# Kernel tuning notes

Hardware: AMD Instinct MI355X
Metric: run time of the kernel (lower is better)

## Reference

```python
import jax, jax.numpy as jnp
import numpy as np

T, B, IN, H = 2048, 2048, 5, 10


def setup_inputs() -> dict:
    key = jax.random.key(0)
    ks = jax.random.split(key, 7)
    return {
        "x": jax.random.normal(ks[0], (T, B, IN), dtype=jnp.float32),
        "hx0": jax.random.uniform(ks[1], (B, H), dtype=jnp.float32),
        "cx0": jax.random.uniform(ks[2], (B, H), dtype=jnp.float32),
        "W_ih": jax.random.normal(ks[3], (4 * H, IN), dtype=jnp.float32) * 0.3,
        "W_hh": jax.random.normal(ks[4], (4 * H, H), dtype=jnp.float32) * 0.3,
        "b_ih": jax.random.normal(ks[5], (4 * H,), dtype=jnp.float32) * 0.1,
        "b_hh": jax.random.normal(ks[6], (4 * H,), dtype=jnp.float32) * 0.1,
    }


def reference(x, hx0, cx0, W_ih, W_hh, b_ih, b_hh):
    # torch.nn.LSTMCell gate order: i, f, g, o
    bias = b_ih + b_hh  # [4H]

    def step(carry, xt):
        h, c = carry  # [B, H] each
        gates = xt @ W_ih.T + h @ W_hh.T + bias  # [B, 4H]
        i, f, g, o = jnp.split(gates, 4, axis=-1)
        c_new = jax.nn.sigmoid(f) * c + jax.nn.sigmoid(i) * jnp.tanh(g)
        h_new = jax.nn.sigmoid(o) * jnp.tanh(c_new)
        return (h_new, c_new), h_new

    _, hs = jax.lax.scan(step, (hx0, cx0), x)  # hs: [T, B, H]
    # original concatenates per-step hx along dim 0 -> [T*B, H]
    return hs.reshape(-1, hs.shape[-1])
```

## Files before the change

### kernel.cpp

```cpp
#include <hip/hip_runtime.h>


#define T_STEPS 2048
#define BATCH   2048
#define NIN     5
#define NH      10
#define PF      8

__device__ __forceinline__ float hw_exp2(float v) { return __builtin_amdgcn_exp2f(v); }
__device__ __forceinline__ float hw_rcp(float v)  { return __builtin_amdgcn_rcpf(v); }

__global__ __launch_bounds__(64) void lstm_fused_kernel(
    const float* __restrict__ x,   const float* __restrict__ hx0,
    const float* __restrict__ cx0, const float* __restrict__ Wih,
    const float* __restrict__ Whh, const float* __restrict__ bih,
    const float* __restrict__ bhh, float* __restrict__ out)
{
    const float LOG2E = 1.4426950408889634f;

    const int lane = threadIdx.x;
    int grp = lane / 20;
    const bool act = (grp < 3);
    if (!act) grp = 2;
    int l2 = lane - grp * 20;
    if (l2 > 19) l2 = 19;
    const int j = l2 >> 1;
    const int p = l2 & 1;

    const int b    = blockIdx.x * 3 + grp;
    const bool bval = act && (b < BATCH);
    const int bl   = (b < BATCH) ? b : (BATCH - 1);

    const int row_a = p ? (2 * NH + j) : (NH + j);
    const int row_b = p ? (3 * NH + j) : j;

    float wa[NIN + NH], wb[NIN + NH];
#pragma unroll
    for (int k = 0; k < NIN; ++k) {
        wa[k] = Wih[row_a * NIN + k];
        wb[k] = Wih[row_b * NIN + k];
    }
#pragma unroll
    for (int k = 0; k < NH; ++k) {
        wa[NIN + k] = Whh[row_a * NH + k];
        wb[NIN + k] = Whh[row_b * NH + k];
    }
    const float bias_a = bih[row_a] + bhh[row_a];
    const float bias_b = bih[row_b] + bhh[row_b];

    const float ka = p ? (-2.0f * LOG2E) : (-LOG2E);
    const float Aa = p ? 2.0f : 1.0f;
    const float Ba = p ? -1.0f : 0.0f;

    float hv[NH];
#pragma unroll
    for (int k = 0; k < NH; ++k) hv[k] = hx0[bl * NH + k];
    float cst = cx0[bl * NH + j];

    const int srcbase = grp * 20;

    const float* xb = x + (size_t)bl * NIN;
    float xr[PF][NIN];
#pragma unroll
    for (int q = 0; q < PF; ++q) {
#pragma unroll
        for (int k = 0; k < NIN; ++k)
            xr[q][k] = xb[(size_t)q * (BATCH * NIN) + k];
    }

    float* outp = out + (size_t)bl * NH + j;
    const bool do_store = bval && (p == 0);

#pragma unroll 1
    for (int t0 = 0; t0 < T_STEPS; t0 += PF) {
#pragma unroll
        for (int q = 0; q < PF; ++q) {
            const int t = t0 + q;

            float a0 = bias_a, a1 = 0.0f, g0 = bias_b, g1 = 0.0f;
            a0 = fmaf(wa[0], xr[q][0], a0);  g0 = fmaf(wb[0], xr[q][0], g0);
            a1 = fmaf(wa[1], xr[q][1], a1);  g1 = fmaf(wb[1], xr[q][1], g1);
            a0 = fmaf(wa[2], xr[q][2], a0);  g0 = fmaf(wb[2], xr[q][2], g0);
            a1 = fmaf(wa[3], xr[q][3], a1);  g1 = fmaf(wb[3], xr[q][3], g1);
            a0 = fmaf(wa[4], xr[q][4], a0);  g0 = fmaf(wb[4], xr[q][4], g0);

            {
                int tn = t + PF;
                if (tn > T_STEPS - 1) tn = T_STEPS - 1;
#pragma unroll
                for (int k = 0; k < NIN; ++k)
                    xr[q][k] = xb[(size_t)tn * (BATCH * NIN) + k];
            }

            a1 = fmaf(wa[5],  hv[0], a1);  g1 = fmaf(wb[5],  hv[0], g1);
            a0 = fmaf(wa[6],  hv[1], a0);  g0 = fmaf(wb[6],  hv[1], g0);
            a1 = fmaf(wa[7],  hv[2], a1);  g1 = fmaf(wb[7],  hv[2], g1);
            a0 = fmaf(wa[8],  hv[3], a0);  g0 = fmaf(wb[8],  hv[3], g0);
            a1 = fmaf(wa[9],  hv[4], a1);  g1 = fmaf(wb[9],  hv[4], g1);
            a0 = fmaf(wa[10], hv[5], a0);  g0 = fmaf(wb[10], hv[5], g0);
            a1 = fmaf(wa[11], hv[6], a1);  g1 = fmaf(wb[11], hv[6], g1);
            a0 = fmaf(wa[12], hv[7], a0);  g0 = fmaf(wb[12], hv[7], g0);
            a1 = fmaf(wa[13], hv[8], a1);  g1 = fmaf(wb[13], hv[8], g1);
            a0 = fmaf(wa[14], hv[9], a0);  g0 = fmaf(wb[14], hv[9], g0);
            const float acc_a = a0 + a1;
            const float acc_b = g0 + g1;

            const float sa = hw_rcp(1.0f + hw_exp2(ka * acc_a));
            const float ya = fmaf(Aa, sa, Ba);
            const float yb = hw_rcp(1.0f + hw_exp2(-LOG2E * acc_b));

            const float tg = __shfl_xor(ya, 1);
            const float so = __shfl_xor(yb, 1);

            cst = fmaf(ya, cst, yb * tg);
            const float tc = fmaf(2.0f, hw_rcp(1.0f + hw_exp2(-2.0f * LOG2E * cst)), -1.0f);
            const float h = so * tc;

            if (do_store) outp[(size_t)t * (BATCH * NH)] = h;

#pragma unroll
            for (int k = 0; k < NH; ++k)
                hv[k] = __shfl(h, srcbase + 2 * k);
        }
    }
}

extern "C" void kernel_launch(void* const* d_in, const int* in_sizes, int n_in,
                              void* d_out, int out_size, void* d_ws, size_t ws_size,
                              hipStream_t stream) {
    const float* x   = (const float*)d_in[0];
    const float* hx0 = (const float*)d_in[1];
    const float* cx0 = (const float*)d_in[2];
    const float* Wih = (const float*)d_in[3];
    const float* Whh = (const float*)d_in[4];
    const float* bih = (const float*)d_in[5];
    const float* bhh = (const float*)d_in[6];
    float* out = (float*)d_out;

    const int nblocks = (BATCH + 2) / 3;
    lstm_fused_kernel<<<nblocks, 64, 0, stream>>>(x, hx0, cx0, Wih, Whh, bih, bhh, out);
}
```

Measured before the change: 790.1 us.

## Map one hidden unit per lane with packed FMA, six batches per wave

Each lane now computes all four gates for one hidden unit, using packed two-wide float math (v2f), instead of splitting gate pairs across two lanes and exchanging them with xor shuffles. Each wave now holds six batch rows instead of three, which halves the number of blocks. The per-step h broadcast uses ds_bpermute directly. Per-lane transcendental and FMA work roughly doubles, traded for removing two shuffles per step and doubling batch throughput per wave on this latency-bound recurrence.

```diff
diff --git a/kernel.cpp b/kernel.cpp
--- a/kernel.cpp
+++ b/kernel.cpp
@@ -6,9 +6,17 @@
 #define NIN     5
 #define NH      10
 #define PF      8
+#define GPW     6
+
+typedef float v2f __attribute__((ext_vector_type(2)));
 
 __device__ __forceinline__ float hw_exp2(float v) { return __builtin_amdgcn_exp2f(v); }
 __device__ __forceinline__ float hw_rcp(float v)  { return __builtin_amdgcn_rcpf(v); }
+__device__ __forceinline__ float bperm_f(int srclane, float v) {
+    return __builtin_bit_cast(float,
+        __builtin_amdgcn_ds_bpermute(srclane << 2, __builtin_bit_cast(int, v)));
+}
+__device__ __forceinline__ v2f splat2(float v) { v2f r; r.x = v; r.y = v; return r; }
 
 __global__ __launch_bounds__(64) void lstm_fused_kernel(
     const float* __restrict__ x,   const float* __restrict__ hx0,
@@ -16,60 +24,52 @@
     const float* __restrict__ Whh, const float* __restrict__ bih,
     const float* __restrict__ bhh, float* __restrict__ out)
 {
-    const float LOG2E = 1.4426950408889634f;
+    const float L2E  = 1.4426950408889634f;
+    const float L2E2 = 2.8853900817779268f;
 
     const int lane = threadIdx.x;
-    int grp = lane / 20;
-    const bool act = (grp < 3);
-    if (!act) grp = 2;
-    int l2 = lane - grp * 20;
-    if (l2 > 19) l2 = 19;
-    const int j = l2 >> 1;
-    const int p = l2 & 1;
+    int grp = lane / NH;
+    if (grp > GPW - 1) grp = GPW - 1;
+    int j = lane - grp * NH;
+    if (j > NH - 1) j = NH - 1;
 
-    const int b    = blockIdx.x * 3 + grp;
-    const bool bval = act && (b < BATCH);
+    const int b    = blockIdx.x * GPW + grp;
+    const bool bval = (lane < GPW * NH) && (b < BATCH);
     const int bl   = (b < BATCH) ? b : (BATCH - 1);
 
-    const int row_a = p ? (2 * NH + j) : (NH + j);
-    const int row_b = p ? (3 * NH + j) : j;
+    const int ri = j, rf = NH + j, rg = 2 * NH + j, ro = 3 * NH + j;
 
-    float wa[NIN + NH], wb[NIN + NH];
+    v2f wxif[NIN], wxgo[NIN], whif[NH], whgo[NH];
 #pragma unroll
     for (int k = 0; k < NIN; ++k) {
-        wa[k] = Wih[row_a * NIN + k];
-        wb[k] = Wih[row_b * NIN + k];
+        wxif[k].x = Wih[ri * NIN + k];  wxif[k].y = Wih[rf * NIN + k];
+        wxgo[k].x = Wih[rg * NIN + k];  wxgo[k].y = Wih[ro * NIN + k];
     }
 #pragma unroll
     for (int k = 0; k < NH; ++k) {
-        wa[NIN + k] = Whh[row_a * NH + k];
-        wb[NIN + k] = Whh[row_b * NH + k];
+        whif[k].x = Whh[ri * NH + k];   whif[k].y = Whh[rf * NH + k];
+        whgo[k].x = Whh[rg * NH + k];   whgo[k].y = Whh[ro * NH + k];
     }
-    const float bias_a = bih[row_a] + bhh[row_a];
-    const float bias_b = bih[row_b] + bhh[row_b];
-
-    const float ka = p ? (-2.0f * LOG2E) : (-LOG2E);
-    const float Aa = p ? 2.0f : 1.0f;
-    const float Ba = p ? -1.0f : 0.0f;
+    v2f bif, bgo;
+    bif.x = bih[ri] + bhh[ri];  bif.y = bih[rf] + bhh[rf];
+    bgo.x = bih[rg] + bhh[rg];  bgo.y = bih[ro] + bhh[ro];
 
     float hv[NH];
 #pragma unroll
     for (int k = 0; k < NH; ++k) hv[k] = hx0[bl * NH + k];
     float cst = cx0[bl * NH + j];
 
-    const int srcbase = grp * 20;
+    const int srcbase = grp * NH;
 
     const float* xb = x + (size_t)bl * NIN;
     float xr[PF][NIN];
 #pragma unroll
-    for (int q = 0; q < PF; ++q) {
+    for (int q = 0; q < PF; ++q)
 #pragma unroll
         for (int k = 0; k < NIN; ++k)
             xr[q][k] = xb[(size_t)q * (BATCH * NIN) + k];
-    }
 
     float* outp = out + (size_t)bl * NH + j;
-    const bool do_store = bval && (p == 0);
 
 #pragma unroll 1
     for (int t0 = 0; t0 < T_STEPS; t0 += PF) {
@@ -77,12 +77,20 @@
         for (int q = 0; q < PF; ++q) {
             const int t = t0 + q;
 
-            float a0 = bias_a, a1 = 0.0f, g0 = bias_b, g1 = 0.0f;
-            a0 = fmaf(wa[0], xr[q][0], a0);  g0 = fmaf(wb[0], xr[q][0], g0);
-            a1 = fmaf(wa[1], xr[q][1], a1);  g1 = fmaf(wb[1], xr[q][1], g1);
-            a0 = fmaf(wa[2], xr[q][2], a0);  g0 = fmaf(wb[2], xr[q][2], g0);
-            a1 = fmaf(wa[3], xr[q][3], a1);  g1 = fmaf(wb[3], xr[q][3], g1);
-            a0 = fmaf(wa[4], xr[q][4], a0);  g0 = fmaf(wb[4], xr[q][4], g0);
+            v2f aif0 = bif, ago0 = bgo;
+            v2f aif1 = splat2(0.0f), ago1 = splat2(0.0f);
+            {
+                v2f xx0 = splat2(xr[q][0]);
+                v2f xx1 = splat2(xr[q][1]);
+                v2f xx2 = splat2(xr[q][2]);
+                v2f xx3 = splat2(xr[q][3]);
+                v2f xx4 = splat2(xr[q][4]);
+                aif0 += xx0 * wxif[0];  ago0 += xx0 * wxgo[0];
+                aif1 += xx1 * wxif[1];  ago1 += xx1 * wxgo[1];
+                aif0 += xx2 * wxif[2];  ago0 += xx2 * wxgo[2];
+                aif1 += xx3 * wxif[3];  ago1 += xx3 * wxgo[3];
+                aif0 += xx4 * wxif[4];  ago0 += xx4 * wxgo[4];
+            }
 
             {
                 int tn = t + PF;
@@ -92,35 +100,30 @@
                     xr[q][k] = xb[(size_t)tn * (BATCH * NIN) + k];
             }
 
-            a1 = fmaf(wa[5],  hv[0], a1);  g1 = fmaf(wb[5],  hv[0], g1);
-            a0 = fmaf(wa[6],  hv[1], a0);  g0 = fmaf(wb[6],  hv[1], g0);
-            a1 = fmaf(wa[7],  hv[2], a1);  g1 = fmaf(wb[7],  hv[2], g1);
-            a0 = fmaf(wa[8],  hv[3], a0);  g0 = fmaf(wb[8],  hv[3], g0);
-            a1 = fmaf(wa[9],  hv[4], a1);  g1 = fmaf(wb[9],  hv[4], g1);
-            a0 = fmaf(wa[10], hv[5], a0);  g0 = fmaf(wb[10], hv[5], g0);
-            a1 = fmaf(wa[11], hv[6], a1);  g1 = fmaf(wb[11], hv[6], g1);
-            a0 = fmaf(wa[12], hv[7], a0);  g0 = fmaf(wb[12], hv[7], g0);
-            a1 = fmaf(wa[13], hv[8], a1);  g1 = fmaf(wb[13], hv[8], g1);
-            a0 = fmaf(wa[14], hv[9], a0);  g0 = fmaf(wb[14], hv[9], g0);
-            const float acc_a = a0 + a1;
-            const float acc_b = g0 + g1;
+#pragma unroll
+            for (int k = 0; k < NH; k += 2) {
+                v2f h0 = splat2(hv[k]);
+                v2f h1 = splat2(hv[k + 1]);
+                aif0 += h0 * whif[k];      ago0 += h0 * whgo[k];
+                aif1 += h1 * whif[k + 1];  ago1 += h1 * whgo[k + 1];
+            }
+            const v2f aif = aif0 + aif1;
+            const v2f ago = ago0 + ago1;
 
-            const float sa = hw_rcp(1.0f + hw_exp2(ka * acc_a));
-            const float ya = fmaf(Aa, sa, Ba);
-            const float yb = hw_rcp(1.0f + hw_exp2(-LOG2E * acc_b));
+            const float si = hw_rcp(1.0f + hw_exp2(-L2E  * aif.x));
+            const float sf = hw_rcp(1.0f + hw_exp2(-L2E  * aif.y));
+            const float tg = fmaf(2.0f, hw_rcp(1.0f + hw_exp2(-L2E2 * ago.x)), -1.0f);
+            const float so = hw_rcp(1.0f + hw_exp2(-L2E  * ago.y));
 
-            const float tg = __shfl_xor(ya, 1);
-            const float so = __shfl_xor(yb, 1);
+            cst = fmaf(sf, cst, si * tg);
+            const float tc = fmaf(2.0f, hw_rcp(1.0f + hw_exp2(-L2E2 * cst)), -1.0f);
+            const float h  = so * tc;
 
-            cst = fmaf(ya, cst, yb * tg);
-            const float tc = fmaf(2.0f, hw_rcp(1.0f + hw_exp2(-2.0f * LOG2E * cst)), -1.0f);
-            const float h = so * tc;
-
-            if (do_store) outp[(size_t)t * (BATCH * NH)] = h;
+            if (bval) outp[(size_t)t * (BATCH * NH)] = h;
 
 #pragma unroll
             for (int k = 0; k < NH; ++k)
-                hv[k] = __shfl(h, srcbase + 2 * k);
+                hv[k] = bperm_f(srcbase + k, h);
         }
     }
 }
@@ -137,6 +140,6 @@
     const float* bhh = (const float*)d_in[6];
     float* out = (float*)d_out;
 
-    const int nblocks = (BATCH + 2) / 3;
+    const int nblocks = (BATCH + GPW - 1) / GPW;
     lstm_fused_kernel<<<nblocks, 64, 0, stream>>>(x, hx0, cx0, Wih, Whh, bih, bhh, out);
 }
```

After: 766.6 us. 1.03x faster.
